# Optimization experiments

Hardware: AMD Instinct MI355X
Metric: run time of the kernel (lower is better)

Reference implementation:

```python
import jax, jax.numpy as jnp
import numpy as np

N_OFFSETS = [(1, 0), (1, 1), (0, 1), (-1, 1), (-1, 0), (-1, -1), (0, -1), (1, -1)]
DILATION = 1


def setup_inputs() -> dict:
    key = jax.random.key(0)
    feats = jax.random.normal(key, (8, 128, 256, 256), dtype=jnp.float32)
    return {"feats": feats}


def reference(feats):
    # feats: [B, C, H, W]
    d = DILATION
    B, C, H, W = feats.shape
    # channel-wise L2 normalize (no eps, matching torch .norm division)
    normed = feats / jnp.linalg.norm(feats, axis=1, keepdims=True)
    # reflect pad last two spatial dims by d
    padded = jnp.pad(normed, ((0, 0), (0, 0), (d, d), (d, d)), mode="reflect")
    # 8 shifted multiply + channel-sum correlations (fixed small offset set)
    corrs = jnp.concatenate(
        [
            jnp.sum(
                normed
                * padded[:, :, d - dx * d // d if False else d - dx:H + d - dx, d - dy:W + d - dy],
                axis=1,
                keepdims=True,
            )
            for dx, dy in [(ox * d, oy * d) for ox, oy in N_OFFSETS]
        ],
        axis=1,
    )  # [B, 8, H, W]
    return corrs
```

## Files before the change

### kernel.cpp

```cpp
#include <hip/hip_runtime.h>


#define BB 8
#define CC 128
#define HH 256
#define WW 256
#define RB 4
#define NSLOT 6
#define PD 10

#define DD(k, j) acc[12 + (k)*4 + (j)]

__global__ __launch_bounds__(256) void featcorr_kernel(
    const float* __restrict__ feats, float* __restrict__ out) {
  const int lane = threadIdx.x;
  const int wy = threadIdx.y;
  const int rb = blockIdx.x;
  const int b = blockIdx.y;
  const int h0 = rb * RB;
  const int h = h0 + wy;

  const size_t HW = (size_t)HH * WW;
  const int col0 = lane * 4;

  __shared__ float lds[PD][NSLOT][WW];

  const int hh1 = h0 - 1 + wy;
  const int sr1 = (hh1 < 0) ? 1 : (hh1 > HH - 1 ? HH - 2 : hh1);
  const float* p1 = feats + (size_t)b * CC * HW + (size_t)sr1 * WW + col0;
  const float* p2 = nullptr;
  if (wy < 2) {
    const int hh2 = h0 - 1 + (4 + wy);
    const int sr2 = (hh2 < 0) ? 1 : (hh2 > HH - 1 ? HH - 2 : hh2);
    p2 = feats + (size_t)b * CC * HW + (size_t)sr2 * WW + col0;
  }

  auto stage = [&](int buf) {
    __builtin_amdgcn_global_load_lds(
        (const __attribute__((address_space(1))) void*)p1,
        (__attribute__((address_space(3))) void*)&lds[buf][wy][0], 16, 0, 0);
    p1 += HW;
    if (wy < 2) {
      __builtin_amdgcn_global_load_lds(
          (const __attribute__((address_space(1))) void*)p2,
          (__attribute__((address_space(3))) void*)&lds[buf][4 + wy][0], 16, 0, 0);
      p2 += HW;
    }
  };

  float acc[44];
#pragma unroll
  for (int a = 0; a < 44; ++a) acc[a] = 0.f;

  auto compute = [&](int buf) {
    const float4 t = *(const float4*)&lds[buf][wy][col0];
    const float4 m = *(const float4*)&lds[buf][wy + 1][col0];
    const float4 bt = *(const float4*)&lds[buf][wy + 2][col0];
    const float rT = __shfl_down(t.x, 1);
    const float rM = __shfl_down(m.x, 1);
    const float rB = __shfl_down(bt.x, 1);
    acc[0] += t.x * t.x;  acc[1] += t.y * t.y;  acc[2] += t.z * t.z;  acc[3] += t.w * t.w;
    acc[4] += m.x * m.x;  acc[5] += m.y * m.y;  acc[6] += m.z * m.z;  acc[7] += m.w * m.w;
    acc[8] += bt.x * bt.x; acc[9] += bt.y * bt.y; acc[10] += bt.z * bt.z; acc[11] += bt.w * bt.w;
    DD(0, 0) += m.x * t.x; DD(0, 1) += m.y * t.y; DD(0, 2) += m.z * t.z; DD(0, 3) += m.w * t.w;
    DD(4, 0) += m.x * bt.x; DD(4, 1) += m.y * bt.y; DD(4, 2) += m.z * bt.z; DD(4, 3) += m.w * bt.w;
    DD(1, 1) += m.y * t.x; DD(1, 2) += m.z * t.y; DD(1, 3) += m.w * t.z;
    DD(1, 0) += rM * t.w;
    DD(2, 1) += m.y * m.x; DD(2, 2) += m.z * m.y; DD(2, 3) += m.w * m.z;
    DD(3, 1) += m.y * bt.x; DD(3, 2) += m.z * bt.y; DD(3, 3) += m.w * bt.z;
    DD(3, 0) += rM * bt.w;
    DD(5, 0) += m.x * bt.y; DD(5, 1) += m.y * bt.z; DD(5, 2) += m.z * bt.w; DD(5, 3) += m.w * rB;
    DD(6, 0) += m.x * m.y; DD(6, 1) += m.y * m.z; DD(6, 2) += m.z * m.w; DD(6, 3) += m.w * rM;
    DD(7, 0) += m.x * t.y; DD(7, 1) += m.y * t.z; DD(7, 2) += m.z * t.w; DD(7, 3) += m.w * rT;
  };

#pragma unroll
  for (int c = 0; c < PD; ++c) stage(c);

  int buf = 0;
  for (int ch = 0; ch < CC; ++ch) {
    if (ch < CC - (PD - 1)) {
      if (wy < 2) {
        asm volatile("s_waitcnt vmcnt(18)" ::: "memory");
      } else {
        asm volatile("s_waitcnt vmcnt(9)" ::: "memory");
      }
    } else {
      asm volatile("s_waitcnt vmcnt(0)" ::: "memory");
    }
    asm volatile("s_barrier" ::: "memory");
    compute(buf);
    asm volatile("s_waitcnt lgkmcnt(0)" ::: "memory");
    asm volatile("s_barrier" ::: "memory");
    if (ch + PD < CC) stage(buf);
    buf = (buf + 1 == PD) ? 0 : buf + 1;
  }

  const float g1 = __shfl_up(DD(1, 0), 1);
  const float g2 = __shfl_up(DD(6, 3), 1);
  const float g3 = __shfl_up(DD(3, 0), 1);
  DD(1, 0) = (lane == 0) ? DD(7, 0) : g1;
  DD(2, 0) = (lane == 0) ? DD(6, 0) : g2;
  DD(3, 0) = (lane == 0) ? DD(5, 0) : g3;
  if (lane == 63) {
    DD(5, 3) = DD(3, 3);
    DD(6, 3) = DD(2, 3);
    DD(7, 3) = DD(1, 3);
  }

  float it[4], im[4], ib[4];
#pragma unroll
  for (int j = 0; j < 4; ++j) {
    it[j] = rsqrtf(acc[j]);
    im[j] = rsqrtf(acc[4 + j]);
    ib[j] = rsqrtf(acc[8 + j]);
  }
  float IT[6], IM[6], IB[6];
  IT[1] = it[0]; IT[2] = it[1]; IT[3] = it[2]; IT[4] = it[3];
  IM[1] = im[0]; IM[2] = im[1]; IM[3] = im[2]; IM[4] = im[3];
  IB[1] = ib[0]; IB[2] = ib[1]; IB[3] = ib[2]; IB[4] = ib[3];
  const float tl = __shfl_up(it[3], 1), ml = __shfl_up(im[3], 1), bl = __shfl_up(ib[3], 1);
  const float tr = __shfl_down(it[0], 1), mr = __shfl_down(im[0], 1), br = __shfl_down(ib[0], 1);
  IT[0] = (lane == 0) ? it[1] : tl;
  IM[0] = (lane == 0) ? im[1] : ml;
  IB[0] = (lane == 0) ? ib[1] : bl;
  IT[5] = (lane == 63) ? it[2] : tr;
  IM[5] = (lane == 63) ? im[2] : mr;
  IB[5] = (lane == 63) ? ib[2] : br;

  float* obase = out + ((size_t)b * 8) * HW + (size_t)h * WW + col0;
#pragma unroll
  for (int k = 0; k < 8; ++k) {
    float v[4];
#pragma unroll
    for (int j = 0; j < 4; ++j) {
      float in;
      switch (k) {
        case 0: in = it[j];     break;
        case 1: in = IT[j];     break;
        case 2: in = IM[j];     break;
        case 3: in = IB[j];     break;
        case 4: in = ib[j];     break;
        case 5: in = IB[j + 2]; break;
        case 6: in = IM[j + 2]; break;
        default: in = IT[j + 2]; break;
      }
      v[j] = DD(k, j) * im[j] * in;
    }
    float4 o;
    o.x = v[0]; o.y = v[1]; o.z = v[2]; o.w = v[3];
    *(float4*)(obase + (size_t)k * HW) = o;
  }
}

extern "C" void kernel_launch(void* const* d_in, const int* in_sizes, int n_in,
                              void* d_out, int out_size, void* d_ws, size_t ws_size,
                              hipStream_t stream) {
  const float* feats = (const float*)d_in[0];
  float* out = (float*)d_out;
  dim3 block(64, RB, 1);
  dim3 grid(HH / RB, BB, 1);
  featcorr_kernel<<<grid, block, 0, stream>>>(feats, out);
}
```

Measured before the change: 370.1 us.

## Use 8-row blocks with a 6-slot LDS ring and a single barrier per channel

```diff
diff --git a/kernel.cpp b/kernel.cpp
--- a/kernel.cpp
+++ b/kernel.cpp
@@ -5,32 +5,34 @@
 #define CC 128
 #define HH 256
 #define WW 256
-#define RB 4
-#define NSLOT 6
-#define PD 10
+#define RB 8
+#define NSLOT (RB + 2)
+#define NBUF 6
+#define PD 5
 
 #define DD(k, j) acc[12 + (k)*4 + (j)]
 
-__global__ __launch_bounds__(256) void featcorr_kernel(
+__global__ __launch_bounds__(512) void featcorr_kernel(
     const float* __restrict__ feats, float* __restrict__ out) {
   const int lane = threadIdx.x;
   const int wy = threadIdx.y;
-  const int rb = blockIdx.x;
   const int b = blockIdx.y;
-  const int h0 = rb * RB;
+  const int h0 = blockIdx.x * RB;
   const int h = h0 + wy;
 
   const size_t HW = (size_t)HH * WW;
   const int col0 = lane * 4;
 
-  __shared__ float lds[PD][NSLOT][WW];
+  __shared__ float lds[NBUF][NSLOT][WW];
+  __shared__ float lds_pad[4];
+  (void)lds_pad;
 
   const int hh1 = h0 - 1 + wy;
   const int sr1 = (hh1 < 0) ? 1 : (hh1 > HH - 1 ? HH - 2 : hh1);
   const float* p1 = feats + (size_t)b * CC * HW + (size_t)sr1 * WW + col0;
   const float* p2 = nullptr;
   if (wy < 2) {
-    const int hh2 = h0 - 1 + (4 + wy);
+    const int hh2 = h0 - 1 + (RB + wy);
     const int sr2 = (hh2 < 0) ? 1 : (hh2 > HH - 1 ? HH - 2 : hh2);
     p2 = feats + (size_t)b * CC * HW + (size_t)sr2 * WW + col0;
   }
@@ -43,7 +45,7 @@
     if (wy < 2) {
       __builtin_amdgcn_global_load_lds(
           (const __attribute__((address_space(1))) void*)p2,
-          (__attribute__((address_space(3))) void*)&lds[buf][4 + wy][0], 16, 0, 0);
+          (__attribute__((address_space(3))) void*)&lds[buf][RB + wy][0], 16, 0, 0);
       p2 += HW;
     }
   };
@@ -77,23 +79,26 @@
 #pragma unroll
   for (int c = 0; c < PD; ++c) stage(c);
 
-  int buf = 0;
-  for (int ch = 0; ch < CC; ++ch) {
-    if (ch < CC - (PD - 1)) {
-      if (wy < 2) {
-        asm volatile("s_waitcnt vmcnt(18)" ::: "memory");
-      } else {
-        asm volatile("s_waitcnt vmcnt(9)" ::: "memory");
-      }
+  int rbuf = 0;
+  int sbuf = PD;
+  for (int ch = 0; ch < CC - PD; ++ch) {
+    if (wy < 2) {
+      asm volatile("s_waitcnt vmcnt(8)" ::: "memory");
     } else {
-      asm volatile("s_waitcnt vmcnt(0)" ::: "memory");
+      asm volatile("s_waitcnt vmcnt(4)" ::: "memory");
     }
     asm volatile("s_barrier" ::: "memory");
-    compute(buf);
-    asm volatile("s_waitcnt lgkmcnt(0)" ::: "memory");
-    asm volatile("s_barrier" ::: "memory");
-    if (ch + PD < CC) stage(buf);
-    buf = (buf + 1 == PD) ? 0 : buf + 1;
+    compute(rbuf);
+    stage(sbuf);
+    rbuf = (rbuf + 1 == NBUF) ? 0 : rbuf + 1;
+    sbuf = (sbuf + 1 == NBUF) ? 0 : sbuf + 1;
+  }
+  asm volatile("s_waitcnt vmcnt(0)" ::: "memory");
+  asm volatile("s_barrier" ::: "memory");
+#pragma unroll
+  for (int k = 0; k < PD; ++k) {
+    compute(rbuf);
+    rbuf = (rbuf + 1 == NBUF) ? 0 : rbuf + 1;
   }
 
   const float g1 = __shfl_up(DD(1, 0), 1);
```

Measured after the change: 357.6 us. -3.4%, faster.
